# Kernel tuning notes

Hardware: AMD Instinct MI355X
Metric: run time of the kernel (lower is better)

Reference implementation:

```python
import jax, jax.numpy as jnp
import numpy as np

N_QUBITS = 10
N_LAYERS = 2
QSVT_DEGREE = 3
DT_RANK = 5  # n_qubits // 2
PI = np.float32(np.pi)

# ---- batched statevector simulation helpers (wire 0 = most significant, as in pennylane default.qubit) ----

def _apply_1q(s, wire, U):
    # s: (batch,) + (2,)*n complex; U: (batch,2,2) or (2,2)
    s = jnp.moveaxis(s, 1 + wire, 1)
    shp = s.shape
    s2 = s.reshape(shp[0], 2, -1)
    if U.ndim == 3:
        out = jnp.einsum('bij,bjr->bir', U, s2)
    else:
        out = jnp.einsum('ij,bjr->bir', U, s2)
    return jnp.moveaxis(out.reshape(shp), 1, 1 + wire)

def _ry(t):
    c = jnp.cos(t / 2).astype(jnp.complex64)
    s = jnp.sin(t / 2).astype(jnp.complex64)
    return jnp.stack([jnp.stack([c, -s], -1), jnp.stack([s, c], -1)], -2)

def _rz(t):
    e = jnp.exp(-0.5j * jnp.asarray(t).astype(jnp.complex64))
    z = jnp.zeros_like(e)
    return jnp.stack([jnp.stack([e, z], -1), jnp.stack([z, jnp.conj(e)], -1)], -2)

def _rx(t):
    c = jnp.cos(t / 2).astype(jnp.complex64)
    s = (-1j) * jnp.sin(t / 2).astype(jnp.complex64)
    return jnp.stack([jnp.stack([c, s], -1), jnp.stack([s, c], -1)], -2)

def _cnot(s, control, target):
    f = jnp.flip(s, axis=1 + target)
    s0 = jax.lax.index_in_dim(s, 0, axis=1 + control, keepdims=True)
    f1 = jax.lax.index_in_dim(f, 1, axis=1 + control, keepdims=True)
    return jnp.concatenate([s0, f1], axis=1 + control)

def _circuit(h, x, dt, cp, pc):
    """Batched selective QSVT circuit; h,x,dt: (B,n). Returns <Z_i> per wire, (B,n) float32."""
    n = N_QUBITS
    b = h.shape[0]
    s = jnp.zeros((b, 2 ** n), jnp.complex64).at[:, 0].set(1.0).reshape((b,) + (2,) * n)
    # 1. state encoding
    for i in range(n):
        s = _apply_1q(s, i, _ry(h[:, i]))
    # 2. delta-modulated QSVT block
    for d in range(QSVT_DEGREE + 1):
        for i in range(n):
            s = _apply_1q(s, i, _rz(pc[d] * dt[:, i] * PI))
        for i in range(n - 1):
            s = _cnot(s, i, i + 1)
        s = _cnot(s, n - 1, 0)
    # 3. variational block
    k = 0
    for _ in range(N_LAYERS):
        for i in range(n):
            s = _apply_1q(s, i, _rx(cp[k]))
            s = _apply_1q(s, i, _ry(cp[k + 1]))
            s = _apply_1q(s, i, _rz(cp[k + 2]))
            k += 3
        for i in range(n - 1):
            s = _cnot(s, i, i + 1)
    # 4. delta-modulated input encoding
    for i in range(n):
        s = _apply_1q(s, i, _ry(x[:, i] * dt[:, i]))
    # 5. <Z_i> measurements
    p = s.real ** 2 + s.imag ** 2
    zs = [(jax.lax.index_in_dim(p, 0, 1 + i, False) - jax.lax.index_in_dim(p, 1, 1 + i, False)).reshape(b, -1).sum(-1) for i in range(n)]
    return jnp.stack(zs, -1).astype(jnp.float32)

def setup_inputs() -> dict:
    key = jax.random.key(0)
    ks = jax.random.split(key, 6)
    B, S, n, r = 128, 512, N_QUBITS, DT_RANK
    angles = jax.random.uniform(ks[0], (B, S, n), jnp.float32) * PI  # angle encoding in [0, pi]
    W_x = jax.random.normal(ks[1], (r + 2 * n, n), jnp.float32) * 0.3  # x_proj weight (no bias)
    W_dt = jax.random.normal(ks[2], (n, r), jnp.float32) * 0.3  # dt_proj weight
    rng = np.random.default_rng(0)
    dt0 = np.exp(rng.random(n) * (np.log(0.1) - np.log(0.001)) + np.log(0.001))
    b_dt = jnp.asarray(dt0 + np.log(-np.expm1(-dt0)), jnp.float32)  # inverse-softplus init
    poly_coeffs = jax.random.normal(ks[3], (QSVT_DEGREE + 1,), jnp.float32) * 0.1
    circuit_params = jax.random.normal(ks[4], (n * N_LAYERS * 3,), jnp.float32) * 0.1
    D = jnp.ones((n,), jnp.float32)
    return {"angles": angles, "W_x": W_x, "W_dt": W_dt, "b_dt": b_dt,
            "poly_coeffs": poly_coeffs, "circuit_params": circuit_params, "D": D}

def reference(angles, W_x, W_dt, b_dt, poly_coeffs, circuit_params, D):
    # selective projections
    x_dbc = jnp.einsum('bsn,kn->bsk', angles, W_x)
    dt_raw = x_dbc[..., :DT_RANK]
    # B slice (x_dbc[..., DT_RANK:DT_RANK+n]) is computed but unused in the original forward
    C = x_dbc[..., DT_RANK + N_QUBITS:]
    dt = jax.nn.softplus(jnp.einsum('bsr,nr->bsn', dt_raw, W_dt) + b_dt)
    dt_angles = jnp.tanh(dt) * PI
    # quantum recurrence uses detached tensors in the original (torch .detach())
    x_sg = jax.lax.stop_gradient(angles)
    dt_sg = jax.lax.stop_gradient(dt_angles)
    cp = jax.lax.stop_gradient(circuit_params)
    pc = jax.lax.stop_gradient(poly_coeffs)

    def step(h, xs):
        x_t, d_t = xs
        h2 = _circuit(h, x_t, d_t, cp, pc)
        return h2, h2

    h0 = jnp.zeros((angles.shape[0], N_QUBITS), jnp.float32)
    _, hs = jax.lax.scan(step, h0, (jnp.swapaxes(x_sg, 0, 1), jnp.swapaxes(dt_sg, 0, 1)))
    hs = jnp.swapaxes(hs, 0, 1)  # (B,S,n)
    return C * hs + D * angles
```

## Files before the change

### kernel.cpp

```cpp
#include <hip/hip_runtime.h>
#include <math.h>


#define PIF 3.14159265358979323846f

constexpr int NQ = 10, SEQ = 512, NB = 128, NTHR = 512;

struct CTbl { int mz[4][NQ]; };
constexpr CTbl build_tbl() {
  CTbl t{};
  unsigned mrow[NQ];
  for (int b = 0; b < NQ; ++b) mrow[b] = 1u << b;
  for (int d = 0; d < 4; ++d) {
    for (int i = 0; i < NQ; ++i) t.mz[d][i] = (int)mrow[9 - i];
    for (int i = 0; i < NQ - 1; ++i) { int bc = 9 - i, bt = 8 - i; mrow[bt] ^= mrow[bc]; }
    mrow[9] ^= mrow[0];
  }
  return t;
}
constexpr CTbl CT = build_tbl();

struct PermCols { int c4[10]; int cL[10]; };
constexpr PermCols build_perms() {
  PermCols P{};
  for (int b = 0; b < 10; ++b) {
    int x = 1 << b;
    for (int d = 0; d < 4; ++d) {
      for (int i = 0; i < 9; ++i) { int bc = 9 - i, bt = 8 - i; if ((x >> bc) & 1) x ^= (1 << bt); }
      if (x & 1) x ^= (1 << 9);
    }
    P.c4[b] = x;
    int y = 1 << b;
    for (int i = 0; i < 9; ++i) { int bc = 9 - i, bt = 8 - i; if ((y >> bc) & 1) y ^= (1 << bt); }
    P.cL[b] = y;
  }
  return P;
}
constexpr PermCols PC = build_perms();

constexpr int lanePart(int x)  { return ((x >> 0) & 1) | (((x >> 5) & 1) << 1) |
                                        (((x >> 1) & 1) << 2) | (((x >> 7) & 1) << 3) |
                                        (((x >> 3) & 1) << 4) | (((x >> 9) & 1) << 5); }
constexpr int wavePart8(int x) { return ((x >> 4) & 1) | (((x >> 8) & 1) << 1) |
                                        (((x >> 6) & 1) << 2); }

constexpr int kmap(int x) {
  return ((x >> 2) & 1)
       | (((x >> 0) & 1) << 1) | (((x >> 5) & 1) << 2) | (((x >> 1) & 1) << 3)
       | (((x >> 7) & 1) << 4) | (((x >> 3) & 1) << 5) | (((x >> 9) & 1) << 6)
       | (((x >> 4) & 1) << 7) | (((x >> 8) & 1) << 8) | (((x >> 6) & 1) << 9);
}
constexpr int swzk(int k) { return k ^ (((k >> 5) & 1) << 1) ^ (((k >> 4) & 1) << 2); }

constexpr int SKC4 = swzk(kmap(PC.c4[2]));
constexpr int SKCL = swzk(kmap(PC.cL[2]));

typedef __attribute__((ext_vector_type(2))) float v2;

template<int C>
__device__ __forceinline__ int dpp1(int x) {
  return __builtin_amdgcn_update_dpp(x, x, C, 0xF, 0xF, false);
}
template<int VL>
__device__ __forceinline__ int lxi(int x) {
  if constexpr (VL == 1)  return dpp1<0xB1>(x);
  else if constexpr (VL == 2)  return dpp1<0x4E>(x);
  else if constexpr (VL == 3)  return dpp1<0x1B>(x);
  else if constexpr (VL <= 7) {
    constexpr int q = (VL & 3) ^ 3;
    int y = x;
    if constexpr (q == 1) y = dpp1<0xB1>(y);
    else if constexpr (q == 2) y = dpp1<0x4E>(y);
    else if constexpr (q == 3) y = dpp1<0x1B>(y);
    return dpp1<0x141>(y);
  } else if constexpr (VL >= 12) {
    constexpr int q = (VL & 3) ^ 3;
    int y = x;
    if constexpr (q == 1) y = dpp1<0xB1>(y);
    else if constexpr (q == 2) y = dpp1<0x4E>(y);
    else if constexpr (q == 3) y = dpp1<0x1B>(y);
    return dpp1<0x140>(y);
  } else {
    constexpr int a = VL & 3;
    int y = x;
    if constexpr (a == 1) y = dpp1<0xB1>(y);
    else if constexpr (a == 2) y = dpp1<0x4E>(y);
    else if constexpr (a == 3) y = dpp1<0x1B>(y);
    y = dpp1<0x141>(y);
    return dpp1<0x140>(y);
  }
}
template<int VL>
__device__ __forceinline__ float lx(float x) {
  if constexpr (VL == 0) return x;
  else if constexpr (VL & 32) {
    int addr = (((int)threadIdx.x & 63) ^ VL) << 2;
    return __int_as_float(__builtin_amdgcn_ds_bpermute(addr, __float_as_int(x)));
  } else if constexpr (VL & 16) {
    return __int_as_float(__builtin_amdgcn_ds_swizzle(__float_as_int(x), (VL << 10) | 0x1F));
  } else {
    return __int_as_float(lxi<VL>(__float_as_int(x)));
  }
}
__device__ __forceinline__ float rdl(float x, int l) {
  return __int_as_float(__builtin_amdgcn_readlane(__float_as_int(x), l));
}

__device__ __forceinline__ void apply2(v2* amp, const v2* p, bool par, float4 U0, float4 U1) {
  v2 u00 = {U0.x, U0.y}, u01 = {U0.z, U0.w}, u10 = {U1.x, U1.y}, u11 = {U1.z, U1.w};
  v2 A = par ? u11 : u00, B = par ? u10 : u01;
  v2 An = {-A.y, A.y}, Bn = {-B.y, B.y};
#pragma unroll
  for (int r = 0; r < 2; ++r) {
    v2 o = amp[r], q = p[r];
    v2 res = A.x * o;
    res += An * __builtin_shufflevector(o, o, 1, 0);
    res += B.x * q;
    res += Bn * __builtin_shufflevector(q, q, 1, 0);
    amp[r] = res;
  }
}

template<int VL>
__device__ __forceinline__ void gate_lane2(v2* amp, float4 U0, float4 U1, int lane) {
  v2 p[2];
#pragma unroll
  for (int r = 0; r < 2; ++r) { p[r].x = lx<VL>(amp[r].x); p[r].y = lx<VL>(amp[r].y); }
  apply2(amp, p, (lane & VL) != 0, U0, U1);
}

__device__ __forceinline__ void gate_reg1(v2* amp, float4 U0, float4 U1) {
  v2 u00 = {U0.x, U0.y}, u01 = {U0.z, U0.w}, u10 = {U1.x, U1.y}, u11 = {U1.z, U1.w};
  v2 o0 = amp[0], o1 = amp[1];
  v2 a0, a1;
  a0.x = u00.x * o0.x - u00.y * o0.y + u01.x * o1.x - u01.y * o1.y;
  a0.y = u00.x * o0.y + u00.y * o0.x + u01.x * o1.y + u01.y * o1.x;
  a1.x = u10.x * o0.x - u10.y * o0.y + u11.x * o1.x - u11.y * o1.y;
  a1.y = u10.x * o0.y + u10.y * o0.x + u11.x * o1.y + u11.y * o1.x;
  amp[0] = a0; amp[1] = a1;
}

template<int VL>
__device__ __forceinline__ float xdot_lane2(const v2* amp) {
  v2 acc = {0.f, 0.f};
#pragma unroll
  for (int r = 0; r < 2; ++r) {
    v2 p; p.x = lx<VL>(amp[r].x); p.y = lx<VL>(amp[r].y);
    acc += amp[r] * p;
  }
  return acc.x + acc.y;
}

__global__ __launch_bounds__(NTHR, 2) void qmamba_main(
    const float* __restrict__ angles, const float* __restrict__ Wx,
    const float* __restrict__ Wdt, const float* __restrict__ bdt,
    const float* __restrict__ pc, const float* __restrict__ cp,
    float* __restrict__ out)
{
  __shared__ __align__(16) float tbl[SEQ][30];
  __shared__ float4 uuL[40];
  __shared__ __align__(16) v2 ex0[1024];
  __shared__ __align__(16) v2 ex1[1024];
  __shared__ float  zb[8][16];

  const int tid  = threadIdx.x;
  const int lane = tid & 63;
  const int wv   = tid >> 6;
  const int b    = blockIdx.x;

  if (tid < 20) {
    int k = tid * 3;
    float al = 0.5f * cp[k], be = 0.5f * cp[k + 1], ga = 0.5f * cp[k + 2];
    float ca = __cosf(al), sa = __sinf(al);
    float cb = __cosf(be), sb = __sinf(be);
    float cg = __cosf(ga), sg = __sinf(ga);
    float2 M00 = make_float2(cb * ca,  sb * sa);
    float2 M01 = make_float2(-sb * ca, -cb * sa);
    float2 M10 = make_float2(sb * ca,  -cb * sa);
    float2 M11 = make_float2(cb * ca,  -sb * sa);
    float2 e0 = make_float2(cg, -sg), e1 = make_float2(cg, sg);
    auto cm = [](float2 a, float2 c) {
      return make_float2(a.x * c.x - a.y * c.y, a.x * c.y + a.y * c.x);
    };
    float2 u00 = cm(M00, e0), u01 = cm(M01, e0), u10 = cm(M10, e1), u11 = cm(M11, e1);
    uuL[2 * tid]     = make_float4(u00.x, u00.y, u01.x, u01.y);
    uuL[2 * tid + 1] = make_float4(u10.x, u10.y, u11.x, u11.y);
  }

  {
    const int t = tid;
    const float* ar = angles + (size_t)(b * SEQ + t) * NQ;
    float a[NQ];
#pragma unroll
    for (int n = 0; n < NQ; ++n) a[n] = ar[n];
    float dtr[5];
#pragma unroll
    for (int r = 0; r < 5; ++r) {
      float acc = 0.f;
#pragma unroll
      for (int n = 0; n < NQ; ++n) acc += a[n] * Wx[r * NQ + n];
      dtr[r] = acc;
    }
    float* rec = &tbl[t][0];
#pragma unroll
    for (int w = 0; w < NQ; ++w) {
      float lin = bdt[w];
#pragma unroll
      for (int r = 0; r < 5; ++r) lin += dtr[r] * Wdt[w * 5 + r];
      float sp = lin > 0.f ? lin + log1pf(__expf(-lin)) : log1pf(__expf(lin));
      float th = tanhf(sp) * PIF;
      float fa = a[w] * th;
      rec[w]      = th;
      rec[10 + w] = __cosf(fa);
      rec[20 + w] = __sinf(fa);
    }
  }
  __syncthreads();

  float pch[4];
#pragma unroll
  for (int d = 0; d < 4; ++d) pch[d] = 0.5f * pc[d] * PIF;

  v2 cw0[8], cw1[8];
  {
    const int s5 = wv & 1, s1 = (wv >> 1) & 1, s3 = (wv >> 2) & 1;
    auto ent = [&](int g, int row, int col) -> v2 {
      float4 R = uuL[2 * g + row];
      return col ? v2{R.z, R.w} : v2{R.x, R.y};
    };
    auto cmul = [](v2 a, v2 c) -> v2 {
      return v2{a.x * c.x - a.y * c.y, a.x * c.y + a.y * c.x};
    };
#pragma unroll
    for (int v = 0; v < 8; ++v) {
      const int v5 = v & 1, v1 = (v >> 1) & 1, v3 = (v >> 2) & 1;
      cw0[v] = cmul(cmul(ent(5,  s5, s5 ^ v5), ent(1,  s1, s1 ^ v1)), ent(3,  s3, s3 ^ v3));
      cw1[v] = cmul(cmul(ent(15, s5, s5 ^ v5), ent(11, s1, s1 ^ v1)), ent(13, s3, s3 ^ v3));
    }
  }

  unsigned PW0 = 0, PW1 = 0;
#pragma unroll
  for (int k = 0; k < 40; ++k) {
    const int m  = CT.mz[k / 10][k % 10];
    const int lm = lanePart(m), wm = wavePart8(m);
    unsigned flip = ((unsigned)((__popc(lane & lm) ^ __popc(wv & wm)) & 1)) ^ 1u;
    if (k < 32) PW0 |= flip << k; else PW1 |= flip << (k - 32);
  }

  int d4k = 0, dLk = 0;
  if (lane & 1)  { d4k ^= kmap(PC.c4[0]); dLk ^= kmap(PC.cL[0]); }
  if (lane & 2)  { d4k ^= kmap(PC.c4[5]); dLk ^= kmap(PC.cL[5]); }
  if (lane & 4)  { d4k ^= kmap(PC.c4[1]); dLk ^= kmap(PC.cL[1]); }
  if (lane & 8)  { d4k ^= kmap(PC.c4[7]); dLk ^= kmap(PC.cL[7]); }
  if (lane & 16) { d4k ^= kmap(PC.c4[3]); dLk ^= kmap(PC.cL[3]); }
  if (lane & 32) { d4k ^= kmap(PC.c4[9]); dLk ^= kmap(PC.cL[9]); }
  if (wv & 1)    { d4k ^= kmap(PC.c4[4]); dLk ^= kmap(PC.cL[4]); }
  if (wv & 2)    { d4k ^= kmap(PC.c4[8]); dLk ^= kmap(PC.cL[8]); }
  if (wv & 4)    { d4k ^= kmap(PC.c4[6]); dLk ^= kmap(PC.cL[6]); }
  const int sd4  = swzk(d4k);
  const int sdL  = swzk(dLk);
  const int sown = swzk((lane << 1) | (wv << 7));

  float hcw[NQ], hsw[NQ];
#pragma unroll
  for (int w = 0; w < NQ; ++w) { hcw[w] = 1.f; hsw[w] = 0.f; }

  v2 amp[2];

#pragma unroll 1
  for (int t = 0; t < SEQ; ++t) {
    float thv[10];
    {
      const float2* rq = (const float2*)&tbl[t][0];
#pragma unroll
      for (int j = 0; j < 5; ++j) { float2 q = rq[j]; thv[2 * j] = q.x; thv[2 * j + 1] = q.y; }
    }

    float F;
    F  = (lane & 1)  ? hsw[9] : hcw[9];
    F *= (lane & 2)  ? hsw[4] : hcw[4];
    F *= (lane & 4)  ? hsw[8] : hcw[8];
    F *= (lane & 8)  ? hsw[2] : hcw[2];
    F *= (lane & 16) ? hsw[6] : hcw[6];
    F *= (lane & 32) ? hsw[0] : hcw[0];
    F *= (wv & 1)    ? hsw[5] : hcw[5];
    F *= (wv & 2)    ? hsw[1] : hcw[1];
    F *= (wv & 4)    ? hsw[3] : hcw[3];
    const float G0 = F * hcw[7];
    const float G1 = F * hsw[7];

    float S0 = 0.f, S1 = 0.f;
#pragma unroll
    for (int k = 0; k < 40; ++k) {
      const int m  = CT.mz[k / 10][k % 10];
      float v = pch[k / 10] * thv[k % 10];
      unsigned fl = ((k < 32 ? (PW0 >> k) : (PW1 >> (k - 32))) & 1u) << 31;
      float sv = __int_as_float(__float_as_int(v) ^ fl);
      if ((m >> 2) & 1) S1 += sv; else S0 += sv;
    }
    {
      float sn, cs;
      __sincosf(S0 + S1, &sn, &cs); amp[0].x = G0 * cs; amp[0].y = G0 * sn;
      __sincosf(S0 - S1, &sn, &cs); amp[1].x = G1 * cs; amp[1].y = G1 * sn;
    }

    ex0[sd4]        = amp[0];
    ex0[sd4 ^ SKC4] = amp[1];
    __syncthreads();
    {
      const float4* q4 = (const float4*)ex0;
      v2 a0 = {0.f, 0.f}, a1 = {0.f, 0.f};
#pragma unroll
      for (int v = 0; v < 8; ++v) {
        float4 q = q4[(sown ^ (v << 7)) >> 1];
        v2 c = cw0[v];
        a0.x += c.x * q.x - c.y * q.y;  a0.y += c.x * q.y + c.y * q.x;
        a1.x += c.x * q.z - c.y * q.w;  a1.y += c.x * q.w + c.y * q.z;
      }
      amp[0] = a0; amp[1] = a1;
    }
    gate_lane2<32>(amp, uuL[0],  uuL[1],  lane);
    gate_lane2<8> (amp, uuL[4],  uuL[5],  lane);
    gate_lane2<2> (amp, uuL[8],  uuL[9],  lane);
    gate_lane2<16>(amp, uuL[12], uuL[13], lane);
    gate_reg1     (amp, uuL[14], uuL[15]);
    gate_lane2<4> (amp, uuL[16], uuL[17], lane);
    gate_lane2<1> (amp, uuL[18], uuL[19], lane);

    ex1[sdL]        = amp[0];
    ex1[sdL ^ SKCL] = amp[1];
    __syncthreads();
    {
      const float4* q4 = (const float4*)ex1;
      v2 a0 = {0.f, 0.f}, a1 = {0.f, 0.f};
#pragma unroll
      for (int v = 0; v < 8; ++v) {
        float4 q = q4[(sown ^ (v << 7)) >> 1];
        v2 c = cw1[v];
        a0.x += c.x * q.x - c.y * q.y;  a0.y += c.x * q.y + c.y * q.x;
        a1.x += c.x * q.z - c.y * q.w;  a1.y += c.x * q.w + c.y * q.z;
      }
      amp[0] = a0; amp[1] = a1;
    }
    gate_lane2<32>(amp, uuL[20], uuL[21], lane);
    gate_lane2<8> (amp, uuL[24], uuL[25], lane);
    gate_lane2<2> (amp, uuL[28], uuL[29], lane);
    gate_lane2<16>(amp, uuL[32], uuL[33], lane);
    gate_reg1     (amp, uuL[34], uuL[35]);
    gate_lane2<4> (amp, uuL[36], uuL[37], lane);
    gate_lane2<1> (amp, uuL[38], uuL[39], lane);

    ex0[sdL]        = amp[0];
    ex0[sdL ^ SKCL] = amp[1];
    __syncthreads();
    v2 pw5[2], pw1[2], pw3[2];
    {
      const float4* q4 = (const float4*)ex0;
      float4 qs = q4[sown >> 1];
      float4 q5 = q4[(sown ^ (1 << 7)) >> 1];
      float4 q1 = q4[(sown ^ (2 << 7)) >> 1];
      float4 q3 = q4[(sown ^ (4 << 7)) >> 1];
      amp[0] = v2{qs.x, qs.y}; amp[1] = v2{qs.z, qs.w};
      pw5[0] = v2{q5.x, q5.y}; pw5[1] = v2{q5.z, q5.w};
      pw1[0] = v2{q1.x, q1.y}; pw1[1] = v2{q1.z, q1.w};
      pw3[0] = v2{q3.x, q3.y}; pw3[1] = v2{q3.z, q3.w};
    }

    float cfv[10], sfv[10];
    {
      const float2* rq = (const float2*)&tbl[t][0];
#pragma unroll
      for (int j = 0; j < 5; ++j) {
        float2 qc = rq[5 + j], qsn = rq[10 + j];
        cfv[2 * j] = qc.x; cfv[2 * j + 1] = qc.y;
        sfv[2 * j] = qsn.x; sfv[2 * j + 1] = qsn.y;
      }
    }

    const float n0 = amp[0].x * amp[0].x + amp[0].y * amp[0].y;
    const float n1 = amp[1].x * amp[1].x + amp[1].y * amp[1].y;
    const float T0 = n0 + n1;
    const float T1 = n0 - n1;

    auto vdot2 = [](const v2* a, const v2* p) {
      v2 acc = a[0] * p[0] + a[1] * p[1];
      return acc.x + acc.y;
    };

    float zv[NQ];
    { float zp = (lane & 32) ? -T0 : T0; zv[0] = cfv[0] * zp - sfv[0] * xdot_lane2<32>(amp); }
    { float zp = (wv & 2)    ? -T0 : T0; zv[1] = cfv[1] * zp - sfv[1] * vdot2(amp, pw1); }
    { float zp = (lane & 8)  ? -T0 : T0; zv[2] = cfv[2] * zp - sfv[2] * xdot_lane2<8>(amp); }
    { float zp = (wv & 4)    ? -T0 : T0; zv[3] = cfv[3] * zp - sfv[3] * vdot2(amp, pw3); }
    { float zp = (lane & 2)  ? -T0 : T0; zv[4] = cfv[4] * zp - sfv[4] * xdot_lane2<2>(amp); }
    { float zp = (wv & 1)    ? -T0 : T0; zv[5] = cfv[5] * zp - sfv[5] * vdot2(amp, pw5); }
    { float zp = (lane & 16) ? -T0 : T0; zv[6] = cfv[6] * zp - sfv[6] * xdot_lane2<16>(amp); }
    { float xr = 2.f * (amp[0].x * amp[1].x + amp[0].y * amp[1].y);
      zv[7] = cfv[7] * T1 - sfv[7] * xr; }
    { float zp = (lane & 4)  ? -T0 : T0; zv[8] = cfv[8] * zp - sfv[8] * xdot_lane2<4>(amp); }
    { float zp = (lane & 1)  ? -T0 : T0; zv[9] = cfv[9] * zp - sfv[9] * xdot_lane2<1>(amp); }

#pragma unroll
    for (int w = 0; w < NQ; ++w) {
      zv[w] += lx<1>(zv[w]);
      zv[w] += lx<2>(zv[w]);
      zv[w] += lx<4>(zv[w]);
    }
    const int l7 = lane & 7;
    float c01 = (l7 & 1) ? zv[1] : zv[0];
    float c23 = (l7 & 1) ? zv[3] : zv[2];
    float c45 = (l7 & 1) ? zv[5] : zv[4];
    float c67 = (l7 & 1) ? zv[7] : zv[6];
    float c03 = (l7 & 2) ? c23 : c01;
    float c47 = (l7 & 2) ? c67 : c45;
    float pk  = (l7 & 4) ? c47 : c03;
    pk += lx<8>(pk);  pk += lx<16>(pk);  pk += lx<32>(pk);
    float z8 = zv[8]; z8 += lx<8>(z8); z8 += lx<16>(z8); z8 += lx<32>(z8);
    float z9 = zv[9]; z9 += lx<8>(z9); z9 += lx<16>(z9); z9 += lx<32>(z9);
    float zsel = pk;
    zsel = (lane == 8) ? z8 : zsel;
    zsel = (lane == 9) ? z9 : zsel;

    if (lane < NQ) zb[wv][lane] = zsel;
    __syncthreads();
    float z = 0.f;
    if (lane < NQ) {
      z = zb[0][lane] + zb[1][lane] + zb[2][lane] + zb[3][lane]
        + zb[4][lane] + zb[5][lane] + zb[6][lane] + zb[7][lane];
      if (wv == 0) out[(size_t)(b * SEQ + t) * NQ + lane] = z;
    }
    float sn_h, cs_h;
    __sincosf(0.5f * z, &sn_h, &cs_h);
#pragma unroll
    for (int w = 0; w < NQ; ++w) { hcw[w] = rdl(cs_h, w); hsw[w] = rdl(sn_h, w); }
  }
}

__global__ __launch_bounds__(256) void qmamba_post(
    const float* __restrict__ angles, const float* __restrict__ Wx,
    const float* __restrict__ Dg, float* __restrict__ out)
{
  int i = blockIdx.x * 256 + threadIdx.x;
  if (i >= NB * SEQ * NQ) return;
  int w  = i % NQ;
  int bt = i / NQ;
  const float* a = angles + (size_t)bt * NQ;
  float C = 0.f;
#pragma unroll
  for (int n = 0; n < NQ; ++n) C += a[n] * Wx[(15 + w) * NQ + n];
  float z = out[i];
  out[i] = C * z + Dg[w] * a[w];
}

extern "C" void kernel_launch(void* const* d_in, const int* in_sizes, int n_in,
                              void* d_out, int out_size, void* d_ws, size_t ws_size,
                              hipStream_t stream) {
  (void)in_sizes; (void)n_in; (void)out_size; (void)d_ws; (void)ws_size;
  const float* angles = (const float*)d_in[0];
  const float* Wx     = (const float*)d_in[1];
  const float* Wdt    = (const float*)d_in[2];
  const float* bdt    = (const float*)d_in[3];
  const float* pc     = (const float*)d_in[4];
  const float* cp     = (const float*)d_in[5];
  const float* Dg     = (const float*)d_in[6];
  float* out = (float*)d_out;
  hipLaunchKernelGGL(qmamba_main, dim3(NB), dim3(NTHR), 0, stream,
                     angles, Wx, Wdt, bdt, pc, cp, out);
  hipLaunchKernelGGL(qmamba_post, dim3((NB * SEQ * NQ + 255) / 256), dim3(256), 0, stream,
                     angles, Wx, Dg, out);
}
```

Baseline: 2.099 ms.

## Precompute per-wire phase coefficients and use permlane swaps for cross-half reductions

The 40-term signed phase accumulation for the QSVT diagonal is folded into per-wire coefficients Kp/Km computed once per thread, so each timestep needs only 10 FMAs per phase instead of 40 sign-flipped adds. Cross-lane exchanges at distances 16 and 32 in reductions and xdot are switched from ds_swizzle/ds_bpermute to the permlane16/32 swap intrinsics, which avoid the LDS path. This costs 20 extra registers per thread, and summing in a different order may change float rounding slightly.

```diff
diff --git a/kernel.cpp b/kernel.cpp
--- a/kernel.cpp
+++ b/kernel.cpp
@@ -90,6 +90,25 @@
     return dpp1<0x140>(y);
   }
 }
+
+template<int VL>
+__device__ __forceinline__ float2 plpair(float x) {
+  int xi = __float_as_int(x);
+  if constexpr (VL == 16) {
+    auto r = __builtin_amdgcn_permlane16_swap(xi, xi, false, false);
+    return make_float2(__int_as_float(r[0]), __int_as_float(r[1]));
+  } else {
+    static_assert(VL == 32, "plpair supports 16/32 only");
+    auto r = __builtin_amdgcn_permlane32_swap(xi, xi, false, false);
+    return make_float2(__int_as_float(r[0]), __int_as_float(r[1]));
+  }
+}
+template<int VL>
+__device__ __forceinline__ float plsum(float x) {
+  float2 p = plpair<VL>(x);
+  return p.x + p.y;
+}
+
 template<int VL>
 __device__ __forceinline__ float lx(float x) {
   if constexpr (VL == 0) return x;
@@ -142,13 +161,24 @@
 
 template<int VL>
 __device__ __forceinline__ float xdot_lane2(const v2* amp) {
-  v2 acc = {0.f, 0.f};
-#pragma unroll
-  for (int r = 0; r < 2; ++r) {
-    v2 p; p.x = lx<VL>(amp[r].x); p.y = lx<VL>(amp[r].y);
-    acc += amp[r] * p;
-  }
-  return acc.x + acc.y;
+  if constexpr (VL == 16 || VL == 32) {
+    float acc = 0.f;
+#pragma unroll
+    for (int r = 0; r < 2; ++r) {
+      float2 px = plpair<VL>(amp[r].x);
+      float2 py = plpair<VL>(amp[r].y);
+      acc += px.x * px.y + py.x * py.y;
+    }
+    return acc;
+  } else {
+    v2 acc = {0.f, 0.f};
+#pragma unroll
+    for (int r = 0; r < 2; ++r) {
+      v2 p; p.x = lx<VL>(amp[r].x); p.y = lx<VL>(amp[r].y);
+      acc += amp[r] * p;
+    }
+    return acc.x + acc.y;
+  }
 }
 
 __global__ __launch_bounds__(NTHR, 2) void qmamba_main(
@@ -217,10 +247,6 @@
   }
   __syncthreads();
 
-  float pch[4];
-#pragma unroll
-  for (int d = 0; d < 4; ++d) pch[d] = 0.5f * pc[d] * PIF;
-
   v2 cw0[8], cw1[8];
   {
     const int s5 = wv & 1, s1 = (wv >> 1) & 1, s3 = (wv >> 2) & 1;
@@ -239,13 +265,25 @@
     }
   }
 
-  unsigned PW0 = 0, PW1 = 0;
-#pragma unroll
-  for (int k = 0; k < 40; ++k) {
-    const int m  = CT.mz[k / 10][k % 10];
-    const int lm = lanePart(m), wm = wavePart8(m);
-    unsigned flip = ((unsigned)((__popc(lane & lm) ^ __popc(wv & wm)) & 1)) ^ 1u;
-    if (k < 32) PW0 |= flip << k; else PW1 |= flip << (k - 32);
+  float Kp[NQ], Km[NQ];
+  {
+    float pch[4];
+#pragma unroll
+    for (int d = 0; d < 4; ++d) pch[d] = 0.5f * pc[d] * PIF;
+#pragma unroll
+    for (int i = 0; i < NQ; ++i) {
+      float k0 = 0.f, k1 = 0.f;
+#pragma unroll
+      for (int d = 0; d < 4; ++d) {
+        const int m  = CT.mz[d][i];
+        const int lm = lanePart(m), wm = wavePart8(m);
+        const int rb = (m >> 2) & 1;
+        const int p0 = (__popc(lane & lm) ^ __popc(wv & wm)) & 1;
+        k0 += p0 ? pch[d] : -pch[d];
+        k1 += (p0 ^ rb) ? pch[d] : -pch[d];
+      }
+      Kp[i] = k0; Km[i] = k1;
+    }
   }
 
   int d4k = 0, dLk = 0;
@@ -290,19 +328,13 @@
     const float G0 = F * hcw[7];
     const float G1 = F * hsw[7];
 
-    float S0 = 0.f, S1 = 0.f;
-#pragma unroll
-    for (int k = 0; k < 40; ++k) {
-      const int m  = CT.mz[k / 10][k % 10];
-      float v = pch[k / 10] * thv[k % 10];
-      unsigned fl = ((k < 32 ? (PW0 >> k) : (PW1 >> (k - 32))) & 1u) << 31;
-      float sv = __int_as_float(__float_as_int(v) ^ fl);
-      if ((m >> 2) & 1) S1 += sv; else S0 += sv;
-    }
+    float Sa = 0.f, Sb = 0.f;
+#pragma unroll
+    for (int i = 0; i < NQ; ++i) { Sa += Kp[i] * thv[i]; Sb += Km[i] * thv[i]; }
     {
       float sn, cs;
-      __sincosf(S0 + S1, &sn, &cs); amp[0].x = G0 * cs; amp[0].y = G0 * sn;
-      __sincosf(S0 - S1, &sn, &cs); amp[1].x = G1 * cs; amp[1].y = G1 * sn;
+      __sincosf(Sa, &sn, &cs); amp[0].x = G0 * cs; amp[0].y = G0 * sn;
+      __sincosf(Sb, &sn, &cs); amp[1].x = G1 * cs; amp[1].y = G1 * sn;
     }
 
     ex0[sd4]        = amp[0];
@@ -415,9 +447,9 @@
     float c03 = (l7 & 2) ? c23 : c01;
     float c47 = (l7 & 2) ? c67 : c45;
     float pk  = (l7 & 4) ? c47 : c03;
-    pk += lx<8>(pk);  pk += lx<16>(pk);  pk += lx<32>(pk);
-    float z8 = zv[8]; z8 += lx<8>(z8); z8 += lx<16>(z8); z8 += lx<32>(z8);
-    float z9 = zv[9]; z9 += lx<8>(z9); z9 += lx<16>(z9); z9 += lx<32>(z9);
+    pk += lx<8>(pk);  pk = plsum<16>(pk);  pk = plsum<32>(pk);
+    float z8 = zv[8]; z8 += lx<8>(z8); z8 = plsum<16>(z8); z8 = plsum<32>(z8);
+    float z9 = zv[9]; z9 += lx<8>(z9); z9 = plsum<16>(z9); z9 = plsum<32>(z9);
     float zsel = pk;
     zsel = (lane == 8) ? z8 : zsel;
     zsel = (lane == 9) ? z9 : zsel;
```

After: 2.116 ms. No clear change (+0.8%).
